# Kernel tuning notes

Measured on AMD Instinct MI355X. Metric: run time of the kernel, lower is better.

Reference implementation:

```python
import jax, jax.numpy as jnp
import numpy as np

N, E, NODE_IN, EDGE_IN, HID, HEADS = 50000, 800000, 64, 32, 64, 2


def setup_inputs() -> dict:
    key = jax.random.key(0)
    ks = jax.random.split(key, 24)
    p = lambda k, shape: (jax.random.normal(k, shape, jnp.float32) * 0.05)
    return {
        "x": jax.random.normal(ks[0], (N, NODE_IN), jnp.float32),
        "edge_index": jax.random.randint(ks[1], (2, E), 0, N),
        "edge_attr": jax.random.normal(ks[2], (E, EDGE_IN), jnp.float32),
        # encoders
        "Wn": p(ks[3], (NODE_IN, HID)), "bn": jnp.zeros((HID,), jnp.float32),
        "We": p(ks[4], (EDGE_IN, HID)), "be": jnp.zeros((HID,), jnp.float32),
        # conv1 (heads=1)
        "W1": p(ks[5], (HID, HID)), "as1": p(ks[6], (1, HID)), "ad1": p(ks[7], (1, HID)),
        "We1": p(ks[8], (HID, HID)), "ae1": p(ks[9], (1, HID)),
        "Wr1": p(ks[10], (HID, HID)), "b1": jnp.zeros((HID,), jnp.float32),
        # conv2 (heads=HEADS)
        "W2": p(ks[11], (HID, HEADS * HID)), "as2": p(ks[12], (HEADS, HID)), "ad2": p(ks[13], (HEADS, HID)),
        "We2": p(ks[14], (HID, HEADS * HID)), "ae2": p(ks[15], (HEADS, HID)),
        "Wr2": p(ks[16], (HID, HEADS * HID)), "b2": jnp.zeros((HEADS * HID,), jnp.float32),
        # output head
        "Wl": p(ks[17], (HEADS * HID, 1)), "bl": jnp.zeros((1,), jnp.float32),
    }


def gat_conv(x, src, dst, eattr, W, a_s, a_d, We_, a_e, Wr, b, heads, num_nodes):
    """PyG GATConv (v1) with edge_dim, add_self_loops(fill='mean'), residual."""
    n_edges = src.shape[0]
    # self-loop edge_attr = scatter-mean of incoming edge attrs per node
    cnt = jax.ops.segment_sum(jnp.ones((n_edges,), x.dtype), dst, num_segments=num_nodes)
    loop_attr = jax.ops.segment_sum(eattr, dst, num_segments=num_nodes) / jnp.maximum(cnt, 1.0)[:, None]
    loop = jnp.arange(num_nodes)
    src = jnp.concatenate([src, loop])
    dst = jnp.concatenate([dst, loop])
    eattr = jnp.concatenate([eattr, loop_attr], axis=0)
    C = W.shape[1] // heads
    h = (x @ W).reshape(num_nodes, heads, C)              # [N,H,C]
    e = (eattr @ We_).reshape(-1, heads, C)               # [E',H,C]
    a_src = jnp.sum(h * a_s, axis=-1)                     # [N,H]
    a_dst = jnp.sum(h * a_d, axis=-1)                     # [N,H]
    a_edge = jnp.sum(e * a_e, axis=-1)                    # [E',H]
    logits = jax.nn.leaky_relu(a_src[src] + a_dst[dst] + a_edge, 0.2)
    m = jax.ops.segment_max(logits, dst, num_segments=num_nodes)
    ex = jnp.exp(logits - m[dst])
    denom = jax.ops.segment_sum(ex, dst, num_segments=num_nodes)
    alpha = ex / (denom[dst] + 1e-16)                     # segment softmax over dst
    out = jax.ops.segment_sum(h[src] * alpha[:, :, None], dst, num_segments=num_nodes)
    return out.reshape(num_nodes, heads * C) + x @ Wr + b


def reference(x, edge_index, edge_attr, Wn, bn, We, be,
              W1, as1, ad1, We1, ae1, Wr1, b1,
              W2, as2, ad2, We2, ae2, Wr2, b2, Wl, bl):
    num_nodes = x.shape[0]
    src, dst = edge_index[0], edge_index[1]
    h = x @ Wn + bn
    ea = edge_attr @ We + be
    h = gat_conv(h, src, dst, ea, W1, as1, ad1, We1, ae1, Wr1, b1, 1, num_nodes)
    h = jax.nn.leaky_relu(h, 0.01)  # dropout inactive (eval)
    h = gat_conv(h, src, dst, ea, W2, as2, ad2, We2, ae2, Wr2, b2, HEADS, num_nodes)
    return (h @ Wl + bl).squeeze(1)  # [N]
```

## Files before the change

kernel.cpp:

```cpp
#include <hip/hip_runtime.h>
#include <hip/hip_bf16.h>
#include <math.h>

#define NODE_IN 64
#define EDGE_IN 32
#define HID 64

__device__ __forceinline__ float leaky02(float x){ return x > 0.f ? x : 0.2f*x; }

__device__ __forceinline__ float wredsum(float v){
  #pragma unroll
  for (int o = 32; o > 0; o >>= 1) v += __shfl_xor(v, o);
  return v;
}
__device__ __forceinline__ float wredmax(float v){
  #pragma unroll
  for (int o = 32; o > 0; o >>= 1) v = fmaxf(v, __shfl_xor(v, o));
  return v;
}

__global__ void k_prep(const float* __restrict__ We,  const float* __restrict__ be,
                       const float* __restrict__ We1, const float* __restrict__ ae1,
                       const float* __restrict__ W2,  const float* __restrict__ as2,
                       const float* __restrict__ ad2, const float* __restrict__ We2,
                       const float* __restrict__ ae2, const float* __restrict__ Wr2,
                       const float* __restrict__ b2,  const float* __restrict__ Wl,
                       const float* __restrict__ bl,  float* __restrict__ wc)
{
  __shared__ float ve1[64], ve2a[64], ve2b[64];
  int k = threadIdx.x;
  if (k < 64) {
    float v1=0.f, va=0.f, vb=0.f, sa0=0.f, sa1=0.f, sd0=0.f, sd1=0.f, t0=0.f, t1=0.f, vr=0.f;
    for (int c = 0; c < 64; c++){
      v1  += We1[k*64+c]     * ae1[c];
      va  += We2[k*128+c]    * ae2[c];
      vb  += We2[k*128+64+c] * ae2[64+c];
      sa0 += W2[k*128+c]     * as2[c];
      sa1 += W2[k*128+64+c]  * as2[64+c];
      sd0 += W2[k*128+c]     * ad2[c];
      sd1 += W2[k*128+64+c]  * ad2[64+c];
      t0  += W2[k*128+c]     * Wl[c];
      t1  += W2[k*128+64+c]  * Wl[64+c];
    }
    for (int j = 0; j < 128; j++) vr += Wr2[k*128+j] * Wl[j];
    ve1[k]=v1; ve2a[k]=va; ve2b[k]=vb;
    wc[128+k]=sa0; wc[192+k]=sa1; wc[256+k]=sd0; wc[320+k]=sd1;
    wc[384+k]=t0;  wc[448+k]=t1;  wc[512+k]=vr;
  }
  __syncthreads();
  if (k < 32) {
    float u1=0.f, ua=0.f, ub=0.f;
    for (int kk = 0; kk < 64; kk++){
      float w = We[k*64+kk];
      u1 += w*ve1[kk]; ua += w*ve2a[kk]; ub += w*ve2b[kk];
    }
    wc[k]=u1; wc[32+k]=ua; wc[64+k]=ub;
  }
  if (k == 0) {
    float c1=0.f, ca=0.f, cb=0.f, co=0.f;
    for (int kk = 0; kk < 64; kk++){ c1+=be[kk]*ve1[kk]; ca+=be[kk]*ve2a[kk]; cb+=be[kk]*ve2b[kk]; }
    for (int j = 0; j < 128; j++) co += b2[j]*Wl[j];
    co += bl[0];
    wc[96]=c1; wc[97]=ca; wc[98]=cb; wc[99]=co;
  }
}

__global__ __launch_bounds__(256) void k_edge(const float* __restrict__ eattr,
    const int* __restrict__ src, const int* __restrict__ dst,
    const float* __restrict__ wc,
    float4* __restrict__ etmp, int* __restrict__ cnt, int E)
{
  int e = blockIdx.x*256 + threadIdx.x;
  if (e >= E) return;
  const float4* a4 = (const float4*)(eattr + (size_t)e*EDGE_IN);
  float d1=0.f, da=0.f, db=0.f;
  #pragma unroll
  for (int i = 0; i < 8; i++){
    float4 v = a4[i];
    d1 += v.x*wc[4*i+0]    + v.y*wc[4*i+1]    + v.z*wc[4*i+2]    + v.w*wc[4*i+3];
    da += v.x*wc[32+4*i+0] + v.y*wc[32+4*i+1] + v.z*wc[32+4*i+2] + v.w*wc[32+4*i+3];
    db += v.x*wc[64+4*i+0] + v.y*wc[64+4*i+1] + v.z*wc[64+4*i+2] + v.w*wc[64+4*i+3];
  }
  etmp[e] = make_float4(__int_as_float(src[e]), d1 + wc[96], da + wc[97], db + wc[98]);
  atomicAdd(&cnt[dst[e]], 1);
}

__global__ __launch_bounds__(256) void k_scan1(const int* __restrict__ cnt,
                                               int* __restrict__ bsum, int N)
{
  __shared__ int sh[256];
  int b = blockIdx.x, t = threadIdx.x;
  int i0 = b*1024 + t*4;
  int s = 0;
  #pragma unroll
  for (int q = 0; q < 4; q++){ int i = i0+q; if (i < N) s += cnt[i]; }
  sh[t] = s; __syncthreads();
  for (int off = 128; off > 0; off >>= 1){
    if (t < off) sh[t] += sh[t+off];
    __syncthreads();
  }
  if (t == 0) bsum[b] = sh[0];
}

__global__ __launch_bounds__(1024) void k_scan2(int* __restrict__ bsum, int nb,
                                                int* __restrict__ rowptr, int N)
{
  __shared__ int sh[1024];
  int t = threadIdx.x;
  int v = (t < nb) ? bsum[t] : 0;
  sh[t] = v; __syncthreads();
  for (int off = 1; off < 1024; off <<= 1){
    int u = (t >= off) ? sh[t-off] : 0;
    __syncthreads();
    sh[t] += u;
    __syncthreads();
  }
  if (t < nb) bsum[t] = sh[t] - v;
  if (t == nb-1) rowptr[N] = sh[t];
}

__global__ __launch_bounds__(256) void k_scan3(const int* __restrict__ cnt,
    const int* __restrict__ bsum, int* __restrict__ rowptr,
    int* __restrict__ cursor, int N)
{
  __shared__ int sh[256];
  int b = blockIdx.x, t = threadIdx.x;
  int i0 = b*1024 + t*4;
  int c[4]; int s = 0;
  #pragma unroll
  for (int q = 0; q < 4; q++){ int i = i0+q; c[q] = (i < N) ? cnt[i] : 0; s += c[q]; }
  int own = s;
  sh[t] = s; __syncthreads();
  for (int off = 1; off < 256; off <<= 1){
    int u = (t >= off) ? sh[t-off] : 0;
    __syncthreads();
    sh[t] += u;
    __syncthreads();
  }
  int run = bsum[b] + sh[t] - own;
  #pragma unroll
  for (int q = 0; q < 4; q++){
    int i = i0+q;
    if (i < N){ rowptr[i] = run; cursor[i] = run; run += c[q]; }
  }
}

__global__ __launch_bounds__(256) void k_fill(const int* __restrict__ dst,
    const float4* __restrict__ etmp, int* __restrict__ cursor,
    float4* __restrict__ edata, int E)
{
  int e = blockIdx.x*256 + threadIdx.x;
  if (e >= E) return;
  int d = dst[e];
  int pos = atomicAdd(&cursor[d], 1);
  edata[pos] = etmp[e];
}

__global__ __launch_bounds__(256) void k_node(const float* __restrict__ x,
    const float* __restrict__ Wn, const float* __restrict__ bn,
    const float* __restrict__ W1, const float* __restrict__ as1, const float* __restrict__ ad1,
    const float* __restrict__ Wr1, const float* __restrict__ b1,
    float* __restrict__ h1, float* __restrict__ hr1,
    float* __restrict__ asrc1, float* __restrict__ adst1, int N)
{
  __shared__ float sA[64][68];
  __shared__ float sW0[64][68];
  __shared__ float sW1[64][68];
  __shared__ float sbn[64], sb1[64], sas[64], sad[64];
  int t = threadIdx.x;
  int n0 = blockIdx.x*64;
  for (int idx = t; idx < 64*64; idx += 256){
    int r = idx>>6, c = idx&63;
    int node = n0 + r;
    sA[r][c]  = (node < N) ? x[(size_t)node*64 + c] : 0.f;
    sW0[r][c] = Wn[idx];
    sW1[r][c] = W1[idx];
  }
  if (t < 64){ sbn[t]=bn[t]; sb1[t]=b1[t]; sas[t]=as1[t]; sad[t]=ad1[t]; }
  __syncthreads();

  int i = t>>2, c0 = (t&3)*16;
  float acc[16];
  #pragma unroll
  for (int cc = 0; cc < 16; cc++) acc[cc] = 0.f;
  for (int k = 0; k < 64; k++){
    float xv = sA[i][k];
    #pragma unroll
    for (int cc = 0; cc < 16; cc++) acc[cc] += xv * sW0[k][c0+cc];
  }
  #pragma unroll
  for (int cc = 0; cc < 16; cc++) acc[cc] += sbn[c0+cc];
  __syncthreads();

  #pragma unroll
  for (int cc = 0; cc < 16; cc++) sA[i][c0+cc] = acc[cc];
  for (int idx = t; idx < 64*64; idx += 256){
    int r = idx>>6, c = idx&63;
    sW0[r][c] = Wr1[idx];
  }
  __syncthreads();

  float a1[16], ar[16];
  #pragma unroll
  for (int cc = 0; cc < 16; cc++){ a1[cc]=0.f; ar[cc]=0.f; }
  for (int k = 0; k < 64; k++){
    float hv = sA[i][k];
    #pragma unroll
    for (int cc = 0; cc < 16; cc++){ a1[cc] += hv*sW1[k][c0+cc]; ar[cc] += hv*sW0[k][c0+cc]; }
  }
  #pragma unroll
  for (int cc = 0; cc < 16; cc++) ar[cc] += sb1[c0+cc];

  float ps = 0.f, pd = 0.f;
  #pragma unroll
  for (int cc = 0; cc < 16; cc++){ ps += a1[cc]*sas[c0+cc]; pd += a1[cc]*sad[c0+cc]; }
  ps += __shfl_xor(ps, 1); ps += __shfl_xor(ps, 2);
  pd += __shfl_xor(pd, 1); pd += __shfl_xor(pd, 2);

  int node = n0 + i;
  if (node < N){
    #pragma unroll
    for (int q = 0; q < 4; q++){
      float4 v1 = make_float4(a1[q*4], a1[q*4+1], a1[q*4+2], a1[q*4+3]);
      float4 v2 = make_float4(ar[q*4], ar[q*4+1], ar[q*4+2], ar[q*4+3]);
      *(float4*)&h1 [(size_t)node*64 + c0 + q*4] = v1;
      *(float4*)&hr1[(size_t)node*64 + c0 + q*4] = v2;
    }
    if ((t&3) == 0){ asrc1[node] = ps; adst1[node] = pd; }
  }
}

__global__ __launch_bounds__(256) void k_conv1(const float4* __restrict__ edata,
    const int* __restrict__ rowptr, const float* __restrict__ h1, const float* __restrict__ hr1,
    const float* __restrict__ asrc1, const float* __restrict__ adst1,
    const float* __restrict__ wc, float4* __restrict__ srcvec, float4* __restrict__ nd0,
    float* __restrict__ rres, int N)
{
  int n = (int)((blockIdx.x*blockDim.x + threadIdx.x) >> 6);
  int lane = threadIdx.x & 63;
  if (n >= N) return;
  int base = rowptr[n];
  int deg  = rowptr[n+1] - base;
  float adn = adst1[n], asn = asrc1[n];

  float m = -1e30f, ss1 = 0.f, ssa = 0.f, ssb = 0.f;
  for (int j = lane; j < deg; j += 64){
    float4 ed = edata[base+j];
    int s = __float_as_int(ed.x);
    float l = leaky02(asrc1[s] + adn + ed.y);
    m = fmaxf(m, l); ss1 += ed.y; ssa += ed.z; ssb += ed.w;
  }
  m = wredmax(m); ss1 = wredsum(ss1); ssa = wredsum(ssa); ssb = wredsum(ssb);
  float invdeg = deg > 0 ? 1.f/(float)deg : 0.f;
  float ll = leaky02(asn + adn + ss1*invdeg);
  m = fmaxf(m, ll);

  float den = 0.f;
  for (int j = lane; j < deg; j += 64){
    float4 ed = edata[base+j];
    int s = __float_as_int(ed.x);
    float l = leaky02(asrc1[s] + adn + ed.y);
    den += __expf(l - m);
  }
  den = wredsum(den);
  den += __expf(ll - m);
  float inv = 1.f/(den + 1e-16f);

  float acc = __expf(ll - m)*inv * h1[(size_t)n*64 + lane];
  for (int cs = 0; cs < deg; cs += 64){
    int j = cs + lane;
    float w = 0.f; int s = 0;
    if (j < deg){
      float4 ed = edata[base+j];
      s = __float_as_int(ed.x);
      float l = leaky02(asrc1[s] + adn + ed.y);
      w = __expf(l - m)*inv;
    }
    int kmax = min(64, deg - cs);
    for (int k = 0; k < kmax; k++){
      float wk = __shfl(w, k);
      int   sk = __shfl(s, k);
      acc += wk * h1[(size_t)sk*64 + lane];
    }
  }
  float hA = acc + hr1[(size_t)n*64 + lane];
  hA = hA > 0.f ? hA : 0.01f*hA;

  float d0 = wredsum(hA*wc[128+lane]);
  float d1 = wredsum(hA*wc[192+lane]);
  float d2 = wredsum(hA*wc[256+lane]);
  float d3 = wredsum(hA*wc[320+lane]);
  float d4 = wredsum(hA*wc[384+lane]);
  float d5 = wredsum(hA*wc[448+lane]);
  float d6 = wredsum(hA*wc[512+lane]);
  if (lane == 0){
    srcvec[n] = make_float4(d4, d5, d0, d1);
    nd0[n]    = make_float4(d2, d3, ssa*invdeg, ssb*invdeg);
    rres[n]   = d6;
  }
}

__global__ __launch_bounds__(256) void k_conv2(const float4* __restrict__ edata,
    const int* __restrict__ rowptr, const float4* __restrict__ srcvec,
    const float4* __restrict__ nd0, const float* __restrict__ rres,
    const float* __restrict__ wc, float* __restrict__ out, int N)
{
  int n = (int)((blockIdx.x*blockDim.x + threadIdx.x) >> 6);
  int lane = threadIdx.x & 63;
  if (n >= N) return;
  int base = rowptr[n], deg = rowptr[n+1] - base;
  float4 nd  = nd0[n];
  float4 own = srcvec[n];

  float m0 = -1e30f, m1 = -1e30f;
  for (int j = lane; j < deg; j += 64){
    float4 ed = edata[base+j];
    int s = __float_as_int(ed.x);
    float4 sv = srcvec[s];
    float l0 = leaky02(sv.z + nd.x + ed.z);
    float l1 = leaky02(sv.w + nd.y + ed.w);
    m0 = fmaxf(m0, l0); m1 = fmaxf(m1, l1);
  }
  m0 = wredmax(m0); m1 = wredmax(m1);
  float ll0 = leaky02(own.z + nd.x + nd.z);
  float ll1 = leaky02(own.w + nd.y + nd.w);
  m0 = fmaxf(m0, ll0); m1 = fmaxf(m1, ll1);

  float den0=0.f, den1=0.f, num0=0.f, num1=0.f;
  for (int j = lane; j < deg; j += 64){
    float4 ed = edata[base+j];
    int s = __float_as_int(ed.x);
    float4 sv = srcvec[s];
    float l0 = leaky02(sv.z + nd.x + ed.z);
    float l1 = leaky02(sv.w + nd.y + ed.w);
    float e0 = __expf(l0 - m0), e1 = __expf(l1 - m1);
    den0 += e0; den1 += e1; num0 += e0*sv.x; num1 += e1*sv.y;
  }
  den0 = wredsum(den0); den1 = wredsum(den1);
  num0 = wredsum(num0); num1 = wredsum(num1);
  float e0 = __expf(ll0 - m0), e1 = __expf(ll1 - m1);
  den0 += e0; den1 += e1; num0 += e0*own.x; num1 += e1*own.y;

  if (lane == 0)
    out[n] = num0/(den0+1e-16f) + num1/(den1+1e-16f) + rres[n] + wc[99];
}

extern "C" void kernel_launch(void* const* d_in, const int* in_sizes, int n_in,
                              void* d_out, int out_size, void* d_ws, size_t ws_size,
                              hipStream_t stream)
{
  const float* x     = (const float*)d_in[0];
  const int*   ei    = (const int*)  d_in[1];
  const float* eattr = (const float*)d_in[2];
  const float* Wn  = (const float*)d_in[3];
  const float* bn  = (const float*)d_in[4];
  const float* We  = (const float*)d_in[5];
  const float* be  = (const float*)d_in[6];
  const float* W1  = (const float*)d_in[7];
  const float* as1 = (const float*)d_in[8];
  const float* ad1 = (const float*)d_in[9];
  const float* We1 = (const float*)d_in[10];
  const float* ae1 = (const float*)d_in[11];
  const float* Wr1 = (const float*)d_in[12];
  const float* b1  = (const float*)d_in[13];
  const float* W2  = (const float*)d_in[14];
  const float* as2 = (const float*)d_in[15];
  const float* ad2 = (const float*)d_in[16];
  const float* We2 = (const float*)d_in[17];
  const float* ae2 = (const float*)d_in[18];
  const float* Wr2 = (const float*)d_in[19];
  const float* b2  = (const float*)d_in[20];
  const float* Wl  = (const float*)d_in[21];
  const float* bl  = (const float*)d_in[22];

  int N = in_sizes[0]/NODE_IN;
  int E = in_sizes[2]/EDGE_IN;
  const int* srcArr = ei;
  const int* dstArr = ei + E;

  char* p = (char*)d_ws;
  auto alloc = [&](size_t bytes)->char* { char* r = p; p += (bytes + 255) & ~(size_t)255; return r; };
  float*  wc     = (float*) alloc(1024*4);
  float4* etmp   = (float4*)alloc((size_t)E*16);
  int*    cnt    = (int*)   alloc((size_t)N*4);
  int*    rowptr = (int*)   alloc((size_t)(N+1)*4);
  int*    cursor = (int*)   alloc((size_t)N*4);
  int*    bsum   = (int*)   alloc(4096*4);
  float4* edata  = (float4*)alloc((size_t)E*16);
  float*  h1     = (float*) alloc((size_t)N*HID*4);
  float*  hr1    = (float*) alloc((size_t)N*HID*4);
  float*  asrc1  = (float*) alloc((size_t)N*4);
  float*  adst1  = (float*) alloc((size_t)N*4);
  float4* srcvec = (float4*)alloc((size_t)N*16);
  float4* nd0    = (float4*)alloc((size_t)N*16);
  float*  rres   = (float*) alloc((size_t)N*4);

  int nb = (N + 1023) / 1024;

  hipMemsetAsync(cnt, 0, (size_t)N*4, stream);
  k_prep<<<1, 64, 0, stream>>>(We, be, We1, ae1, W2, as2, ad2, We2, ae2, Wr2, b2, Wl, bl, wc);
  k_edge<<<(E+255)/256, 256, 0, stream>>>(eattr, srcArr, dstArr, wc, etmp, cnt, E);
  k_scan1<<<nb, 256, 0, stream>>>(cnt, bsum, N);
  k_scan2<<<1, 1024, 0, stream>>>(bsum, nb, rowptr, N);
  k_scan3<<<nb, 256, 0, stream>>>(cnt, bsum, rowptr, cursor, N);
  k_fill<<<(E+255)/256, 256, 0, stream>>>(dstArr, etmp, cursor, edata, E);
  k_node<<<(N+63)/64, 256, 0, stream>>>(x, Wn, bn, W1, as1, ad1, Wr1, b1, h1, hr1, asrc1, adst1, N);
  k_conv1<<<(N+3)/4, 256, 0, stream>>>(edata, rowptr, h1, hr1, asrc1, adst1, wc, srcvec, nd0, rres, N);
  k_conv2<<<(N+3)/4, 256, 0, stream>>>(edata, rowptr, srcvec, nd0, rres, wc, (float*)d_out, N);
}
```

Measured before the change: 445.4 us.

## Fuse edge projection into CSR fill, retile node GEMM, single-pass softmax for low degree

After: 417.3 us. 6.3% less time.

```diff
diff --git a/kernel.cpp b/kernel.cpp
--- a/kernel.cpp
+++ b/kernel.cpp
@@ -65,23 +65,11 @@
   }
 }
 
-__global__ __launch_bounds__(256) void k_edge(const float* __restrict__ eattr,
-    const int* __restrict__ src, const int* __restrict__ dst,
-    const float* __restrict__ wc,
-    float4* __restrict__ etmp, int* __restrict__ cnt, int E)
+__global__ __launch_bounds__(256) void k_cnt(const int* __restrict__ dst,
+                                             int* __restrict__ cnt, int E)
 {
   int e = blockIdx.x*256 + threadIdx.x;
   if (e >= E) return;
-  const float4* a4 = (const float4*)(eattr + (size_t)e*EDGE_IN);
-  float d1=0.f, da=0.f, db=0.f;
-  #pragma unroll
-  for (int i = 0; i < 8; i++){
-    float4 v = a4[i];
-    d1 += v.x*wc[4*i+0]    + v.y*wc[4*i+1]    + v.z*wc[4*i+2]    + v.w*wc[4*i+3];
-    da += v.x*wc[32+4*i+0] + v.y*wc[32+4*i+1] + v.z*wc[32+4*i+2] + v.w*wc[32+4*i+3];
-    db += v.x*wc[64+4*i+0] + v.y*wc[64+4*i+1] + v.z*wc[64+4*i+2] + v.w*wc[64+4*i+3];
-  }
-  etmp[e] = make_float4(__int_as_float(src[e]), d1 + wc[96], da + wc[97], db + wc[98]);
   atomicAdd(&cnt[dst[e]], 1);
 }
 
@@ -145,15 +133,25 @@
   }
 }
 
-__global__ __launch_bounds__(256) void k_fill(const int* __restrict__ dst,
-    const float4* __restrict__ etmp, int* __restrict__ cursor,
+__global__ __launch_bounds__(256) void k_edge_fill(const float* __restrict__ eattr,
+    const int* __restrict__ src, const int* __restrict__ dst,
+    const float* __restrict__ wc, int* __restrict__ cursor,
     float4* __restrict__ edata, int E)
 {
   int e = blockIdx.x*256 + threadIdx.x;
   if (e >= E) return;
+  const float4* a4 = (const float4*)(eattr + (size_t)e*EDGE_IN);
+  float d1=0.f, da=0.f, db=0.f;
+  #pragma unroll
+  for (int i = 0; i < 8; i++){
+    float4 v = a4[i];
+    d1 += v.x*wc[4*i+0]    + v.y*wc[4*i+1]    + v.z*wc[4*i+2]    + v.w*wc[4*i+3];
+    da += v.x*wc[32+4*i+0] + v.y*wc[32+4*i+1] + v.z*wc[32+4*i+2] + v.w*wc[32+4*i+3];
+    db += v.x*wc[64+4*i+0] + v.y*wc[64+4*i+1] + v.z*wc[64+4*i+2] + v.w*wc[64+4*i+3];
+  }
   int d = dst[e];
   int pos = atomicAdd(&cursor[d], 1);
-  edata[pos] = etmp[e];
+  edata[pos] = make_float4(__int_as_float(src[e]), d1 + wc[96], da + wc[97], db + wc[98]);
 }
 
 __global__ __launch_bounds__(256) void k_node(const float* __restrict__ x,
@@ -163,70 +161,101 @@
     float* __restrict__ h1, float* __restrict__ hr1,
     float* __restrict__ asrc1, float* __restrict__ adst1, int N)
 {
-  __shared__ float sA[64][68];
-  __shared__ float sW0[64][68];
-  __shared__ float sW1[64][68];
+  __shared__ float sA[128][65];
+  __shared__ float sW[64][64];
   __shared__ float sbn[64], sb1[64], sas[64], sad[64];
   int t = threadIdx.x;
-  int n0 = blockIdx.x*64;
-  for (int idx = t; idx < 64*64; idx += 256){
+  int n0 = blockIdx.x*128;
+  int i = t>>2, c0 = (t&3)*16;
+  int nA = n0 + i, nB = n0 + 64 + i;
+
+  for (int idx = t; idx < 128*64; idx += 256){
     int r = idx>>6, c = idx&63;
     int node = n0 + r;
-    sA[r][c]  = (node < N) ? x[(size_t)node*64 + c] : 0.f;
-    sW0[r][c] = Wn[idx];
-    sW1[r][c] = W1[idx];
-  }
+    sA[r][c] = (node < N) ? x[(size_t)node*64 + c] : 0.f;
+  }
+  for (int idx = t; idx < 64*64; idx += 256) sW[idx>>6][idx&63] = Wn[idx];
   if (t < 64){ sbn[t]=bn[t]; sb1[t]=b1[t]; sas[t]=as1[t]; sad[t]=ad1[t]; }
   __syncthreads();
 
-  int i = t>>2, c0 = (t&3)*16;
-  float acc[16];
-  #pragma unroll
-  for (int cc = 0; cc < 16; cc++) acc[cc] = 0.f;
+  float hA[16], hB[16];
+  #pragma unroll
+  for (int cc = 0; cc < 16; cc++){ hA[cc]=0.f; hB[cc]=0.f; }
   for (int k = 0; k < 64; k++){
-    float xv = sA[i][k];
-    #pragma unroll
-    for (int cc = 0; cc < 16; cc++) acc[cc] += xv * sW0[k][c0+cc];
-  }
-  #pragma unroll
-  for (int cc = 0; cc < 16; cc++) acc[cc] += sbn[c0+cc];
-  __syncthreads();
-
-  #pragma unroll
-  for (int cc = 0; cc < 16; cc++) sA[i][c0+cc] = acc[cc];
-  for (int idx = t; idx < 64*64; idx += 256){
-    int r = idx>>6, c = idx&63;
-    sW0[r][c] = Wr1[idx];
-  }
-  __syncthreads();
-
-  float a1[16], ar[16];
-  #pragma unroll
-  for (int cc = 0; cc < 16; cc++){ a1[cc]=0.f; ar[cc]=0.f; }
+    float xa = sA[i][k], xb = sA[i+64][k];
+    #pragma unroll
+    for (int cc = 0; cc < 16; cc++){
+      float w = sW[k][c0+cc];
+      hA[cc] += xa*w; hB[cc] += xb*w;
+    }
+  }
+  #pragma unroll
+  for (int cc = 0; cc < 16; cc++){ hA[cc] += sbn[c0+cc]; hB[cc] += sbn[c0+cc]; }
+  #pragma unroll
+  for (int cc = 0; cc < 16; cc++){ sA[i][c0+cc] = hA[cc]; sA[i+64][c0+cc] = hB[cc]; }
+  __syncthreads();
+  for (int idx = t; idx < 64*64; idx += 256) sW[idx>>6][idx&63] = W1[idx];
+  __syncthreads();
+
+  float a1A[16], a1B[16];
+  #pragma unroll
+  for (int cc = 0; cc < 16; cc++){ a1A[cc]=0.f; a1B[cc]=0.f; }
   for (int k = 0; k < 64; k++){
-    float hv = sA[i][k];
-    #pragma unroll
-    for (int cc = 0; cc < 16; cc++){ a1[cc] += hv*sW1[k][c0+cc]; ar[cc] += hv*sW0[k][c0+cc]; }
-  }
-  #pragma unroll
-  for (int cc = 0; cc < 16; cc++) ar[cc] += sb1[c0+cc];
-
-  float ps = 0.f, pd = 0.f;
-  #pragma unroll
-  for (int cc = 0; cc < 16; cc++){ ps += a1[cc]*sas[c0+cc]; pd += a1[cc]*sad[c0+cc]; }
-  ps += __shfl_xor(ps, 1); ps += __shfl_xor(ps, 2);
-  pd += __shfl_xor(pd, 1); pd += __shfl_xor(pd, 2);
-
-  int node = n0 + i;
-  if (node < N){
-    #pragma unroll
-    for (int q = 0; q < 4; q++){
-      float4 v1 = make_float4(a1[q*4], a1[q*4+1], a1[q*4+2], a1[q*4+3]);
-      float4 v2 = make_float4(ar[q*4], ar[q*4+1], ar[q*4+2], ar[q*4+3]);
-      *(float4*)&h1 [(size_t)node*64 + c0 + q*4] = v1;
-      *(float4*)&hr1[(size_t)node*64 + c0 + q*4] = v2;
-    }
-    if ((t&3) == 0){ asrc1[node] = ps; adst1[node] = pd; }
+    float ha = sA[i][k], hb = sA[i+64][k];
+    #pragma unroll
+    for (int cc = 0; cc < 16; cc++){
+      float w = sW[k][c0+cc];
+      a1A[cc] += ha*w; a1B[cc] += hb*w;
+    }
+  }
+  float psA=0.f, pdA=0.f, psB=0.f, pdB=0.f;
+  #pragma unroll
+  for (int cc = 0; cc < 16; cc++){
+    psA += a1A[cc]*sas[c0+cc]; pdA += a1A[cc]*sad[c0+cc];
+    psB += a1B[cc]*sas[c0+cc]; pdB += a1B[cc]*sad[c0+cc];
+  }
+  psA += __shfl_xor(psA,1); psA += __shfl_xor(psA,2);
+  pdA += __shfl_xor(pdA,1); pdA += __shfl_xor(pdA,2);
+  psB += __shfl_xor(psB,1); psB += __shfl_xor(psB,2);
+  pdB += __shfl_xor(pdB,1); pdB += __shfl_xor(pdB,2);
+  if (nA < N){
+    #pragma unroll
+    for (int q = 0; q < 4; q++)
+      *(float4*)&h1[(size_t)nA*64 + c0 + q*4] = make_float4(a1A[q*4],a1A[q*4+1],a1A[q*4+2],a1A[q*4+3]);
+    if ((t&3)==0){ asrc1[nA]=psA; adst1[nA]=pdA; }
+  }
+  if (nB < N){
+    #pragma unroll
+    for (int q = 0; q < 4; q++)
+      *(float4*)&h1[(size_t)nB*64 + c0 + q*4] = make_float4(a1B[q*4],a1B[q*4+1],a1B[q*4+2],a1B[q*4+3]);
+    if ((t&3)==0){ asrc1[nB]=psB; adst1[nB]=pdB; }
+  }
+  __syncthreads();
+  for (int idx = t; idx < 64*64; idx += 256) sW[idx>>6][idx&63] = Wr1[idx];
+  __syncthreads();
+
+  float arA[16], arB[16];
+  #pragma unroll
+  for (int cc = 0; cc < 16; cc++){ arA[cc]=0.f; arB[cc]=0.f; }
+  for (int k = 0; k < 64; k++){
+    float ha = sA[i][k], hb = sA[i+64][k];
+    #pragma unroll
+    for (int cc = 0; cc < 16; cc++){
+      float w = sW[k][c0+cc];
+      arA[cc] += ha*w; arB[cc] += hb*w;
+    }
+  }
+  if (nA < N){
+    #pragma unroll
+    for (int q = 0; q < 4; q++)
+      *(float4*)&hr1[(size_t)nA*64 + c0 + q*4] = make_float4(arA[q*4]+sb1[c0+q*4], arA[q*4+1]+sb1[c0+q*4+1],
+                                                             arA[q*4+2]+sb1[c0+q*4+2], arA[q*4+3]+sb1[c0+q*4+3]);
+  }
+  if (nB < N){
+    #pragma unroll
+    for (int q = 0; q < 4; q++)
+      *(float4*)&hr1[(size_t)nB*64 + c0 + q*4] = make_float4(arB[q*4]+sb1[c0+q*4], arB[q*4+1]+sb1[c0+q*4+1],
+                                                             arB[q*4+2]+sb1[c0+q*4+2], arB[q*4+3]+sb1[c0+q*4+3]);
   }
 }
 
@@ -241,58 +270,84 @@
   if (n >= N) return;
   int base = rowptr[n];
   int deg  = rowptr[n+1] - base;
+  float h1n  = h1 [(size_t)n*64 + lane];
+  float hr1n = hr1[(size_t)n*64 + lane];
   float adn = adst1[n], asn = asrc1[n];
-
-  float m = -1e30f, ss1 = 0.f, ssa = 0.f, ssb = 0.f;
-  for (int j = lane; j < deg; j += 64){
-    float4 ed = edata[base+j];
-    int s = __float_as_int(ed.x);
-    float l = leaky02(asrc1[s] + adn + ed.y);
-    m = fmaxf(m, l); ss1 += ed.y; ssa += ed.z; ssb += ed.w;
-  }
-  m = wredmax(m); ss1 = wredsum(ss1); ssa = wredsum(ssa); ssb = wredsum(ssb);
   float invdeg = deg > 0 ? 1.f/(float)deg : 0.f;
-  float ll = leaky02(asn + adn + ss1*invdeg);
-  m = fmaxf(m, ll);
-
-  float den = 0.f;
-  for (int j = lane; j < deg; j += 64){
-    float4 ed = edata[base+j];
-    int s = __float_as_int(ed.x);
-    float l = leaky02(asrc1[s] + adn + ed.y);
-    den += __expf(l - m);
-  }
-  den = wredsum(den);
-  den += __expf(ll - m);
-  float inv = 1.f/(den + 1e-16f);
-
-  float acc = __expf(ll - m)*inv * h1[(size_t)n*64 + lane];
-  for (int cs = 0; cs < deg; cs += 64){
-    int j = cs + lane;
-    float w = 0.f; int s = 0;
-    if (j < deg){
+
+  float acc, ssa, ssb;
+
+  if (deg <= 64){
+    bool has = lane < deg;
+    float4 ed = has ? edata[base+lane] : make_float4(0.f,0.f,0.f,0.f);
+    int s = has ? __float_as_int(ed.x) : n;
+    float l = has ? leaky02(asrc1[s] + adn + ed.y) : -1e30f;
+    float m = wredmax(l);
+    float ss1 = wredsum(ed.y); ssa = wredsum(ed.z); ssb = wredsum(ed.w);
+    float ll = leaky02(asn + adn + ss1*invdeg);
+    m = fmaxf(m, ll);
+    float w = has ? __expf(l - m) : 0.f;
+    float den = wredsum(w) + __expf(ll - m);
+    float inv = 1.f/(den + 1e-16f);
+    w *= inv;
+
+    acc = __expf(ll - m)*inv * h1n;
+    for (int kk = 0; kk < deg; kk += 8){
+      float ww[8]; int ss[8]; float v[8];
+      #pragma unroll
+      for (int q = 0; q < 8; q++){ ww[q] = __shfl(w, kk+q); ss[q] = __shfl(s, kk+q); }
+      #pragma unroll
+      for (int q = 0; q < 8; q++) v[q] = h1[(size_t)ss[q]*64 + lane];
+      #pragma unroll
+      for (int q = 0; q < 8; q++) acc += ww[q]*v[q];
+    }
+  } else {
+    float m = -1e30f, ss1 = 0.f; ssa = 0.f; ssb = 0.f;
+    for (int j = lane; j < deg; j += 64){
       float4 ed = edata[base+j];
-      s = __float_as_int(ed.x);
+      int s = __float_as_int(ed.x);
       float l = leaky02(asrc1[s] + adn + ed.y);
-      w = __expf(l - m)*inv;
-    }
-    int kmax = min(64, deg - cs);
-    for (int k = 0; k < kmax; k++){
-      float wk = __shfl(w, k);
-      int   sk = __shfl(s, k);
-      acc += wk * h1[(size_t)sk*64 + lane];
-    }
-  }
-  float hA = acc + hr1[(size_t)n*64 + lane];
-  hA = hA > 0.f ? hA : 0.01f*hA;
-
-  float d0 = wredsum(hA*wc[128+lane]);
-  float d1 = wredsum(hA*wc[192+lane]);
-  float d2 = wredsum(hA*wc[256+lane]);
-  float d3 = wredsum(hA*wc[320+lane]);
-  float d4 = wredsum(hA*wc[384+lane]);
-  float d5 = wredsum(hA*wc[448+lane]);
-  float d6 = wredsum(hA*wc[512+lane]);
+      m = fmaxf(m, l); ss1 += ed.y; ssa += ed.z; ssb += ed.w;
+    }
+    m = wredmax(m); ss1 = wredsum(ss1); ssa = wredsum(ssa); ssb = wredsum(ssb);
+    float ll = leaky02(asn + adn + ss1*invdeg);
+    m = fmaxf(m, ll);
+    float den = 0.f;
+    for (int j = lane; j < deg; j += 64){
+      float4 ed = edata[base+j];
+      int s = __float_as_int(ed.x);
+      den += __expf(leaky02(asrc1[s] + adn + ed.y) - m);
+    }
+    den = wredsum(den) + __expf(ll - m);
+    float inv = 1.f/(den + 1e-16f);
+    acc = __expf(ll - m)*inv * h1n;
+    for (int cs = 0; cs < deg; cs += 64){
+      int j = cs + lane;
+      float w = 0.f; int s = n;
+      if (j < deg){
+        float4 ed = edata[base+j];
+        s = __float_as_int(ed.x);
+        w = __expf(leaky02(asrc1[s] + adn + ed.y) - m)*inv;
+      }
+      int kmax = min(64, deg - cs);
+      for (int k = 0; k < kmax; k++){
+        float wk = __shfl(w, k);
+        int   sk = __shfl(s, k);
+        acc += wk * h1[(size_t)sk*64 + lane];
+      }
+    }
+  }
+
+  float hAv = acc + hr1n;
+  hAv = hAv > 0.f ? hAv : 0.01f*hAv;
+
+  float d0 = wredsum(hAv*wc[128+lane]);
+  float d1 = wredsum(hAv*wc[192+lane]);
+  float d2 = wredsum(hAv*wc[256+lane]);
+  float d3 = wredsum(hAv*wc[320+lane]);
+  float d4 = wredsum(hAv*wc[384+lane]);
+  float d5 = wredsum(hAv*wc[448+lane]);
+  float d6 = wredsum(hAv*wc[512+lane]);
   if (lane == 0){
     srcvec[n] = make_float4(d4, d5, d0, d1);
     nd0[n]    = make_float4(d2, d3, ssa*invdeg, ssb*invdeg);
@@ -311,38 +366,57 @@
   int base = rowptr[n], deg = rowptr[n+1] - base;
   float4 nd  = nd0[n];
   float4 own = srcvec[n];
-
-  float m0 = -1e30f, m1 = -1e30f;
-  for (int j = lane; j < deg; j += 64){
-    float4 ed = edata[base+j];
-    int s = __float_as_int(ed.x);
+  float rn = rres[n];
+
+  float num0, num1, den0, den1, m0, m1;
+
+  if (deg <= 64){
+    bool has = lane < deg;
+    float4 ed = has ? edata[base+lane] : make_float4(0.f,0.f,0.f,0.f);
+    int s = has ? __float_as_int(ed.x) : n;
     float4 sv = srcvec[s];
-    float l0 = leaky02(sv.z + nd.x + ed.z);
-    float l1 = leaky02(sv.w + nd.y + ed.w);
-    m0 = fmaxf(m0, l0); m1 = fmaxf(m1, l1);
-  }
-  m0 = wredmax(m0); m1 = wredmax(m1);
-  float ll0 = leaky02(own.z + nd.x + nd.z);
-  float ll1 = leaky02(own.w + nd.y + nd.w);
-  m0 = fmaxf(m0, ll0); m1 = fmaxf(m1, ll1);
-
-  float den0=0.f, den1=0.f, num0=0.f, num1=0.f;
-  for (int j = lane; j < deg; j += 64){
-    float4 ed = edata[base+j];
-    int s = __float_as_int(ed.x);
-    float4 sv = srcvec[s];
-    float l0 = leaky02(sv.z + nd.x + ed.z);
-    float l1 = leaky02(sv.w + nd.y + ed.w);
-    float e0 = __expf(l0 - m0), e1 = __expf(l1 - m1);
-    den0 += e0; den1 += e1; num0 += e0*sv.x; num1 += e1*sv.y;
-  }
-  den0 = wredsum(den0); den1 = wredsum(den1);
-  num0 = wredsum(num0); num1 = wredsum(num1);
-  float e0 = __expf(ll0 - m0), e1 = __expf(ll1 - m1);
-  den0 += e0; den1 += e1; num0 += e0*own.x; num1 += e1*own.y;
+    float l0 = has ? leaky02(sv.z + nd.x + ed.z) : -1e30f;
+    float l1 = has ? leaky02(sv.w + nd.y + ed.w) : -1e30f;
+    m0 = wredmax(l0); m1 = wredmax(l1);
+    float ll0 = leaky02(own.z + nd.x + nd.z);
+    float ll1 = leaky02(own.w + nd.y + nd.w);
+    m0 = fmaxf(m0, ll0); m1 = fmaxf(m1, ll1);
+    float e0 = has ? __expf(l0 - m0) : 0.f;
+    float e1 = has ? __expf(l1 - m1) : 0.f;
+    den0 = wredsum(e0); den1 = wredsum(e1);
+    num0 = wredsum(e0*sv.x); num1 = wredsum(e1*sv.y);
+    float se0 = __expf(ll0 - m0), se1 = __expf(ll1 - m1);
+    den0 += se0; den1 += se1; num0 += se0*own.x; num1 += se1*own.y;
+  } else {
+    m0 = -1e30f; m1 = -1e30f;
+    for (int j = lane; j < deg; j += 64){
+      float4 ed = edata[base+j];
+      int s = __float_as_int(ed.x);
+      float4 sv = srcvec[s];
+      m0 = fmaxf(m0, leaky02(sv.z + nd.x + ed.z));
+      m1 = fmaxf(m1, leaky02(sv.w + nd.y + ed.w));
+    }
+    m0 = wredmax(m0); m1 = wredmax(m1);
+    float ll0 = leaky02(own.z + nd.x + nd.z);
+    float ll1 = leaky02(own.w + nd.y + nd.w);
+    m0 = fmaxf(m0, ll0); m1 = fmaxf(m1, ll1);
+    den0=0.f; den1=0.f; num0=0.f; num1=0.f;
+    for (int j = lane; j < deg; j += 64){
+      float4 ed = edata[base+j];
+      int s = __float_as_int(ed.x);
+      float4 sv = srcvec[s];
+      float e0 = __expf(leaky02(sv.z + nd.x + ed.z) - m0);
+      float e1 = __expf(leaky02(sv.w + nd.y + ed.w) - m1);
+      den0 += e0; den1 += e1; num0 += e0*sv.x; num1 += e1*sv.y;
+    }
+    den0 = wredsum(den0); den1 = wredsum(den1);
+    num0 = wredsum(num0); num1 = wredsum(num1);
+    float se0 = __expf(ll0 - m0), se1 = __expf(ll1 - m1);
+    den0 += se0; den1 += se1; num0 += se0*own.x; num1 += se1*own.y;
+  }
 
   if (lane == 0)
-    out[n] = num0/(den0+1e-16f) + num1/(den1+1e-16f) + rres[n] + wc[99];
+    out[n] = num0/(den0+1e-16f) + num1/(den1+1e-16f) + rn + wc[99];
 }
 
 extern "C" void kernel_launch(void* const* d_in, const int* in_sizes, int n_in,
@@ -381,7 +455,6 @@
   char* p = (char*)d_ws;
   auto alloc = [&](size_t bytes)->char* { char* r = p; p += (bytes + 255) & ~(size_t)255; return r; };
   float*  wc     = (float*) alloc(1024*4);
-  float4* etmp   = (float4*)alloc((size_t)E*16);
   int*    cnt    = (int*)   alloc((size_t)N*4);
   int*    rowptr = (int*)   alloc((size_t)(N+1)*4);
   int*    cursor = (int*)   alloc((size_t)N*4);
@@ -399,12 +472,12 @@
 
   hipMemsetAsync(cnt, 0, (size_t)N*4, stream);
   k_prep<<<1, 64, 0, stream>>>(We, be, We1, ae1, W2, as2, ad2, We2, ae2, Wr2, b2, Wl, bl, wc);
-  k_edge<<<(E+255)/256, 256, 0, stream>>>(eattr, srcArr, dstArr, wc, etmp, cnt, E);
+  k_cnt<<<(E+255)/256, 256, 0, stream>>>(dstArr, cnt, E);
   k_scan1<<<nb, 256, 0, stream>>>(cnt, bsum, N);
   k_scan2<<<1, 1024, 0, stream>>>(bsum, nb, rowptr, N);
   k_scan3<<<nb, 256, 0, stream>>>(cnt, bsum, rowptr, cursor, N);
-  k_fill<<<(E+255)/256, 256, 0, stream>>>(dstArr, etmp, cursor, edata, E);
-  k_node<<<(N+63)/64, 256, 0, stream>>>(x, Wn, bn, W1, as1, ad1, Wr1, b1, h1, hr1, asrc1, adst1, N);
+  k_edge_fill<<<(E+255)/256, 256, 0, stream>>>(eattr, srcArr, dstArr, wc, cursor, edata, E);
+  k_node<<<(N+127)/128, 256, 0, stream>>>(x, Wn, bn, W1, as1, ad1, Wr1, b1, h1, hr1, asrc1, adst1, N);
   k_conv1<<<(N+3)/4, 256, 0, stream>>>(edata, rowptr, h1, hr1, asrc1, adst1, wc, srcvec, nd0, rres, N);
   k_conv2<<<(N+3)/4, 256, 0, stream>>>(edata, rowptr, srcvec, nd0, rres, wc, (float*)d_out, N);
 }
```
